# Kernel optimization log

Hardware: AMD Instinct MI355X
Metric: run time of the kernel (lower is better)

## Reference

```python
import jax, jax.numpy as jnp
import numpy as np

B, IN, H = 4096, 1024, 1024


def setup_inputs() -> dict:
    key = jax.random.key(0)
    ks = jax.random.split(key, 6)
    s_h = 1.0 / np.sqrt(H)
    s_x = 1.0 / np.sqrt(IN)
    return {
        "x": jax.random.normal(ks[0], (B, IN), jnp.float32),
        "h": jax.random.normal(ks[1], (B, H), jnp.float32),
        "c": jax.random.normal(ks[2], (B, H), jnp.float32),
        # hidden_lin: Linear(H, 4H) with bias
        "Wh": jax.random.uniform(ks[3], (4 * H, H), jnp.float32, -s_h, s_h),
        "bh": jax.random.uniform(ks[4], (4 * H,), jnp.float32, -s_h, s_h),
        # input_lin: Linear(IN, 4H), bias=False
        "Wx": jax.random.uniform(ks[5], (4 * H, IN), jnp.float32, -s_x, s_x),
    }


def reference(x, h, c, Wh, bh, Wx):
    # ifgo = h @ Wh^T + bh + x @ Wx^T   -> [B, 4H]
    ifgo = jnp.dot(h, Wh.T) + bh + jnp.dot(x, Wx.T)
    i, f, g, o = jnp.split(ifgo, 4, axis=1)
    i = jax.nn.sigmoid(i)
    f = jax.nn.sigmoid(f)
    g = jnp.tanh(g)
    o = jax.nn.sigmoid(o)
    c_next = f * c + i * g
    h_next = o * jnp.tanh(c_next)
    return (h_next, c_next)
```

## Files before the change

### kernel.cpp

```cpp
#include <hip/hip_runtime.h>
#include <cstdint>
#include <cstddef>


#define NB   4096
#define KH   1024
#define KK   2048
#define ARR_ELEMS 4194304

typedef __bf16 bf16x8 __attribute__((ext_vector_type(8)));
typedef float  f32x4  __attribute__((ext_vector_type(4)));

__device__ inline unsigned short f2bf(float f) {
    union { float f; unsigned int u; } v; v.f = f;
    unsigned int u = v.u;
    u += 0x7FFFu + ((u >> 16) & 1u);
    return (unsigned short)(u >> 16);
}

__device__ inline float fsig(float v)  { return __builtin_amdgcn_rcpf(1.f + __expf(-v)); }
__device__ inline float ftanh(float v) { return 1.f - 2.f * __builtin_amdgcn_rcpf(1.f + __expf(2.f * v)); }

__global__ void convert_kernel(const float* __restrict__ h, const float* __restrict__ x,
                               const float* __restrict__ Wh, const float* __restrict__ Wx,
                               unsigned short* __restrict__ A, unsigned short* __restrict__ W) {
    int idx = blockIdx.x * 256 + threadIdx.x;
    int arr = idx >> 20;
    int off = (idx & 0xFFFFF) << 2;
    const float* src = (arr == 0) ? h : (arr == 1) ? x : (arr == 2) ? Wh : Wx;
    float4 v = *(const float4*)(src + off);
    unsigned int lo = (unsigned int)f2bf(v.x) | ((unsigned int)f2bf(v.y) << 16);
    unsigned int hi = (unsigned int)f2bf(v.z) | ((unsigned int)f2bf(v.w) << 16);
    uint2 packed; packed.x = lo; packed.y = hi;

    int row = off >> 10;
    int col = off & 1023;
    unsigned short* dst;
    size_t dstOff;
    if (arr < 2) {
        dst = A;
        dstOff = (size_t)row * KK + (arr == 1 ? 1024 : 0) + col;
    } else {
        int g = row >> 10, j = row & 1023;
        int p = ((j >> 4) << 6) | (g << 4) | (j & 15);
        dst = W;
        dstOff = (size_t)p * KK + (arr == 3 ? 1024 : 0) + col;
    }
    *(uint2*)(dst + dstOff) = packed;
}

__global__ void gemm_kernel(const unsigned short* __restrict__ A,
                            const unsigned short* __restrict__ W,
                            const float* __restrict__ bh,
                            const float* __restrict__ c,
                            float* __restrict__ out) {
    __shared__ __align__(16) unsigned short As[2 * 128 * 32];
    __shared__ __align__(16) unsigned short Bs[2 * 128 * 32];

    const int tid  = threadIdx.x;
    const int wave = tid >> 6;
    const int lane = tid & 63;
    const int tileN = blockIdx.x;
    const int tileM = blockIdx.y;

    const int stRow  = wave * 16 + (lane >> 2);
    const int stColE = (lane & 3) * 8;
    const unsigned short* gaBase = A + (size_t)(tileM * 128 + stRow) * KK + stColE;
    const unsigned short* gbBase = W + (size_t)(tileN * 128 + stRow) * KK + stColE;

    const int mBase = (wave >> 1) * 64;
    const int nBase = (wave & 1) * 64;
    const int fr = lane & 15;
    const int fk = (lane >> 4) * 8;

    f32x4 acc[4][4] = {};

    for (int kt = 0; kt < 32; ++kt) {
        const unsigned short* ga = gaBase + kt * 64;
        const unsigned short* gb = gbBase + kt * 64;
        #pragma unroll
        for (int i = 0; i < 4; ++i) {
            const int gOff = (i & 1) * 64 * KK + (i >> 1) * 32;
            const int lOff = i * 2048 + wave * 512;
            __builtin_amdgcn_global_load_lds(
                (const __attribute__((address_space(1))) void*)(ga + gOff),
                (__attribute__((address_space(3))) void*)(As + lOff), 16, 0, 0);
            __builtin_amdgcn_global_load_lds(
                (const __attribute__((address_space(1))) void*)(gb + gOff),
                (__attribute__((address_space(3))) void*)(Bs + lOff), 16, 0, 0);
        }

        __syncthreads();

        #pragma unroll
        for (int s = 0; s < 2; ++s) {
            bf16x8 a[4], b[4];
            #pragma unroll
            for (int i = 0; i < 4; ++i)
                a[i] = *(const bf16x8*)(As + s * 4096 + (mBase + i * 16 + fr) * 32 + fk);
            #pragma unroll
            for (int j = 0; j < 4; ++j)
                b[j] = *(const bf16x8*)(Bs + s * 4096 + (nBase + j * 16 + fr) * 32 + fk);

            #pragma unroll
            for (int i = 0; i < 4; ++i)
                #pragma unroll
                for (int j = 0; j < 4; ++j)
                    acc[i][j] = __builtin_amdgcn_mfma_f32_16x16x32_bf16(a[i], b[j], acc[i][j], 0, 0, 0);
        }

        __syncthreads();
    }

    const int j = ((tileN * 2 + (wave & 1)) << 4) | (lane & 15);
    const float bi = bh[j];
    const float bf = bh[j + 1024];
    const float bg = bh[j + 2048];
    const float bo = bh[j + 3072];

    const int row0 = tileM * 128 + mBase + (lane >> 4) * 4;

    float cv[4][4];
    #pragma unroll
    for (int i = 0; i < 4; ++i)
        #pragma unroll
        for (int r = 0; r < 4; ++r)
            cv[i][r] = c[(size_t)(row0 + i * 16 + r) * KH + j];

    #pragma unroll
    for (int i = 0; i < 4; ++i) {
        #pragma unroll
        for (int r = 0; r < 4; ++r) {
            const size_t idx = (size_t)(row0 + i * 16 + r) * KH + j;
            float iv = fsig(acc[i][0][r] + bi);
            float fv = fsig(acc[i][1][r] + bf);
            float gv = ftanh(acc[i][2][r] + bg);
            float ov = fsig(acc[i][3][r] + bo);
            float cn = fv * cv[i][r] + iv * gv;
            float hn = ov * ftanh(cn);
            out[idx] = hn;
            out[(size_t)ARR_ELEMS + idx] = cn;
        }
    }
}

extern "C" void kernel_launch(void* const* d_in, const int* in_sizes, int n_in,
                              void* d_out, int out_size, void* d_ws, size_t ws_size,
                              hipStream_t stream) {
    const float* x  = (const float*)d_in[0];
    const float* h  = (const float*)d_in[1];
    const float* c  = (const float*)d_in[2];
    const float* Wh = (const float*)d_in[3];
    const float* bh = (const float*)d_in[4];
    const float* Wx = (const float*)d_in[5];
    float* out = (float*)d_out;

    unsigned short* ws   = (unsigned short*)d_ws;
    unsigned short* Acat = ws;
    unsigned short* Wcat = ws + 2 * (size_t)ARR_ELEMS;

    convert_kernel<<<16384, 256, 0, stream>>>(h, x, Wh, Wx, Acat, Wcat);
    dim3 grid(32, 32);
    gemm_kernel<<<grid, 256, 0, stream>>>(Acat, Wcat, bh, c, out);
}
```

Before: 202.4 us.

## Double-buffer LDS K-tiles and use fragment-native LDS layout in GEMM

The GEMM main loop now uses two LDS buffers of 32-wide K slices, so the next slice is prefetched with global_load_lds while the current one is consumed by MFMA. This replaces the old load, sync, compute, sync pattern, which stalled on every tile. Tiles are stored in LDS in the order each MFMA fragment reads them, so each lane does a contiguous 16-byte read and bank conflicts should drop. The trade-off is half as much K per iteration, giving twice as many barriers and smaller global loads per step.

```diff
diff --git a/kernel.cpp b/kernel.cpp
--- a/kernel.cpp
+++ b/kernel.cpp
@@ -54,8 +54,8 @@
                             const float* __restrict__ bh,
                             const float* __restrict__ c,
                             float* __restrict__ out) {
-    __shared__ __align__(16) unsigned short As[2 * 128 * 32];
-    __shared__ __align__(16) unsigned short Bs[2 * 128 * 32];
+    __shared__ __align__(16) unsigned short As[2 * 4096];
+    __shared__ __align__(16) unsigned short Bs[2 * 4096];
 
     const int tid  = threadIdx.x;
     const int wave = tid >> 6;
@@ -63,54 +63,50 @@
     const int tileN = blockIdx.x;
     const int tileM = blockIdx.y;
 
-    const int stRow  = wave * 16 + (lane >> 2);
-    const int stColE = (lane & 3) * 8;
-    const unsigned short* gaBase = A + (size_t)(tileM * 128 + stRow) * KK + stColE;
-    const unsigned short* gbBase = W + (size_t)(tileN * 128 + stRow) * KK + stColE;
+    const unsigned short* gaB = A + (size_t)(tileM * 128 + wave * 16 + (lane & 15)) * KK + (lane >> 4) * 8;
+    const unsigned short* gbB = W + (size_t)(tileN * 128 + wave * 16 + (lane & 15)) * KK + (lane >> 4) * 8;
 
-    const int mBase = (wave >> 1) * 64;
-    const int nBase = (wave & 1) * 64;
-    const int fr = lane & 15;
-    const int fk = (lane >> 4) * 8;
+    const int mg = (wave >> 1) * 4;
+    const int ng = (wave & 1) * 4;
 
     f32x4 acc[4][4] = {};
 
-    for (int kt = 0; kt < 32; ++kt) {
-        const unsigned short* ga = gaBase + kt * 64;
-        const unsigned short* gb = gbBase + kt * 64;
+#define STAGE(kt, buf) do {                                                        \
+        const unsigned short* ga_ = gaB + (kt) * 32;                               \
+        const unsigned short* gb_ = gbB + (kt) * 32;                               \
+        _Pragma("unroll")                                                          \
+        for (int s_ = 0; s_ < 2; ++s_) {                                           \
+            __builtin_amdgcn_global_load_lds(                                      \
+                (const __attribute__((address_space(1))) void*)(ga_ + (size_t)s_ * 64 * KK), \
+                (__attribute__((address_space(3))) void*)(As + (buf) * 4096 + (s_ * 4 + wave) * 512), 16, 0, 0); \
+            __builtin_amdgcn_global_load_lds(                                      \
+                (const __attribute__((address_space(1))) void*)(gb_ + (size_t)s_ * 64 * KK), \
+                (__attribute__((address_space(3))) void*)(Bs + (buf) * 4096 + (s_ * 4 + wave) * 512), 16, 0, 0); \
+        }                                                                          \
+    } while (0)
+
+    STAGE(0, 0);
+
+    for (int kt = 0; kt < 64; ++kt) {
+        const int p = kt & 1;
+        __syncthreads();
+        if (kt < 63) STAGE(kt + 1, p ^ 1);
+
+        bf16x8 a[4], b[4];
         #pragma unroll
-        for (int i = 0; i < 4; ++i) {
-            const int gOff = (i & 1) * 64 * KK + (i >> 1) * 32;
-            const int lOff = i * 2048 + wave * 512;
-            __builtin_amdgcn_global_load_lds(
-                (const __attribute__((address_space(1))) void*)(ga + gOff),
-                (__attribute__((address_space(3))) void*)(As + lOff), 16, 0, 0);
-            __builtin_amdgcn_global_load_lds(
-                (const __attribute__((address_space(1))) void*)(gb + gOff),
-                (__attribute__((address_space(3))) void*)(Bs + lOff), 16, 0, 0);
-        }
-
-        __syncthreads();
+        for (int i = 0; i < 4; ++i)
+            a[i] = *(const bf16x8*)(As + p * 4096 + (mg + i) * 512 + lane * 8);
+        #pragma unroll
+        for (int j = 0; j < 4; ++j)
+            b[j] = *(const bf16x8*)(Bs + p * 4096 + (ng + j) * 512 + lane * 8);
 
         #pragma unroll
-        for (int s = 0; s < 2; ++s) {
-            bf16x8 a[4], b[4];
-            #pragma unroll
-            for (int i = 0; i < 4; ++i)
-                a[i] = *(const bf16x8*)(As + s * 4096 + (mBase + i * 16 + fr) * 32 + fk);
+        for (int i = 0; i < 4; ++i)
             #pragma unroll
             for (int j = 0; j < 4; ++j)
-                b[j] = *(const bf16x8*)(Bs + s * 4096 + (nBase + j * 16 + fr) * 32 + fk);
-
-            #pragma unroll
-            for (int i = 0; i < 4; ++i)
-                #pragma unroll
-                for (int j = 0; j < 4; ++j)
-                    acc[i][j] = __builtin_amdgcn_mfma_f32_16x16x32_bf16(a[i], b[j], acc[i][j], 0, 0, 0);
-        }
-
-        __syncthreads();
+                acc[i][j] = __builtin_amdgcn_mfma_f32_16x16x32_bf16(a[i], b[j], acc[i][j], 0, 0, 0);
     }
+#undef STAGE
 
     const int j = ((tileN * 2 + (wave & 1)) << 4) | (lane & 15);
     const float bi = bh[j];
@@ -118,7 +114,7 @@
     const float bg = bh[j + 2048];
     const float bo = bh[j + 3072];
 
-    const int row0 = tileM * 128 + mBase + (lane >> 4) * 4;
+    const int row0 = tileM * 128 + (wave >> 1) * 64 + (lane >> 4) * 4;
 
     float cv[4][4];
     #pragma unroll
```

Result: slower. 259.3 us (+28.1%).
